# Kernel tuning notes

Hardware: AMD Instinct MI355X
Metric: run time of the kernel (lower is better)

Reference implementation:

```python
import jax, jax.numpy as jnp
import numpy as np

LEAKY_SLOPE = 0.01  # torch nn.LeakyReLU default

def _mlp(x, w1, b1, w2, b2):
    # MLP_Layer(num_layers=2, batch_norm=False): Linear -> ReLU -> Linear
    return jax.nn.relu(x @ w1 + b1) @ w2 + b2

def _edge_softmax(scores, dst, num_nodes):
    # softmax over incoming edges of each destination node; scores: [E, H]
    m = jax.ops.segment_max(scores, dst, num_segments=num_nodes)  # [N, H]
    e = jnp.exp(scores - m[dst])
    s = jax.ops.segment_sum(e, dst, num_segments=num_nodes)       # [N, H]
    return e / s[dst]

def setup_inputs() -> dict:
    key = jax.random.key(0)
    ks = jax.random.split(key, 10)
    N, E, H = 50000, 800000, 4
    D_H, PCA, PI, HID = 64, 64, 32, 128
    inp = {
        "h":    jax.random.normal(ks[0], (N, D_H), jnp.float32),
        "pca":  jax.random.normal(ks[1], (N, PCA), jnp.float32),
        "pimg": jax.random.normal(ks[2], (N, PI), jnp.float32),
        "pca_w1": jax.random.normal(ks[3], (2 * PCA, HID), jnp.float32) * (1.0 / np.sqrt(2 * PCA)),
        "pca_b1": jnp.zeros((HID,), jnp.float32),
        "pca_w2": jax.random.normal(ks[4], (HID, H), jnp.float32) * (1.0 / np.sqrt(HID)),
        "pca_b2": jnp.zeros((H,), jnp.float32),
        "pi_w1": jax.random.normal(ks[5], (2 * PI, HID), jnp.float32) * (1.0 / np.sqrt(2 * PI)),
        "pi_b1": jnp.zeros((HID,), jnp.float32),
        "pi_w2": jax.random.normal(ks[6], (HID, H), jnp.float32) * (1.0 / np.sqrt(HID)),
        "pi_b2": jnp.zeros((H,), jnp.float32),
        "src": jax.random.randint(ks[7], (E,), 0, N, jnp.int32),
        "dst": jax.random.randint(ks[8], (E,), 0, N, jnp.int32),
    }
    return inp

def reference(h, pca, pimg, pca_w1, pca_b1, pca_w2, pca_b2,
              pi_w1, pi_b1, pi_w2, pi_b2, src, dst):
    N = h.shape[0]

    def attend(feat, w1, b1, w2, b2):
        e_feat = jnp.concatenate([feat[src], feat[dst]], axis=1)        # [E, 2F]
        score = jax.nn.leaky_relu(_mlp(e_feat, w1, b1, w2, b2), LEAKY_SLOPE)  # [E, H]
        a = _edge_softmax(score, dst, N)                                # [E, H]
        msg = h[src][:, None, :] * a[:, :, None]                        # [E, H, D]
        return jax.ops.segment_sum(msg, dst, num_segments=N)           # [N, H, D]

    out_pca = attend(pca, pca_w1, pca_b1, pca_w2, pca_b2)
    out_pi = attend(pimg, pi_w1, pi_b1, pi_w2, pi_b2)
    return jnp.concatenate([out_pca, out_pi], axis=-1)                  # [N, H, 2D]
```

## Files before the change

### kernel.cpp

```cpp
#include <hip/hip_runtime.h>
#include <hip/hip_fp16.h>

constexpr int HID = 128;
constexpr int DH  = 64;

typedef _Float16 f16x2 __attribute__((ext_vector_type(2)));
typedef _Float16 fh8   __attribute__((ext_vector_type(8)));
typedef float    f32x4v __attribute__((ext_vector_type(4)));

__device__ __forceinline__ fh8 relu8(fh8 x) {
  fh8 z = {0, 0, 0, 0, 0, 0, 0, 0};
#if __has_builtin(__builtin_elementwise_max)
  return __builtin_elementwise_max(x, z);
#else
  fh8 r;
#pragma unroll
  for (int i = 0; i < 8; i++) r[i] = x[i] > z[i] ? x[i] : z[i];
  return r;
#endif
}

template<int F, int NB>
__launch_bounds__(256)
__global__ void uv_kernel(const float* __restrict__ feat, const float* __restrict__ w1,
                          const float* __restrict__ b1,
                          _Float16* __restrict__ u_cat, _Float16* __restrict__ v_cat,
                          int roff, int N) {
  __shared__ float sfeat[NB][F + 1];
  int nb = blockIdx.x * NB;
  for (int i = threadIdx.x; i < NB * F; i += 256) {
    int n = i / F, k = i - n * F;
    int gn = nb + n;
    sfeat[n][k] = (gn < N) ? feat[(size_t)gn * F + k] : 0.f;
  }
  __syncthreads();
  int j = threadIdx.x & 127;
  int g = threadIdx.x >> 7;
  constexpr int NPT = NB / 2;
  float ua[NPT], va[NPT];
#pragma unroll
  for (int i = 0; i < NPT; i++) { ua[i] = 0.f; va[i] = 0.f; }
  for (int k = 0; k < F; k++) {
    float wu = w1[k * HID + j];
    float wv = w1[(F + k) * HID + j];
#pragma unroll
    for (int i = 0; i < NPT; i++) {
      float f = sfeat[g * NPT + i][k];
      ua[i] = fmaf(f, wu, ua[i]);
      va[i] = fmaf(f, wv, va[i]);
    }
  }
  float b1v = b1[j];
#pragma unroll
  for (int i = 0; i < NPT; i++) {
    int gn = nb + g * NPT + i;
    if (gn < N) {
      u_cat[(size_t)gn * 256 + roff + j] = (_Float16)ua[i];
      v_cat[(size_t)gn * 256 + roff + j] = (_Float16)(va[i] + b1v);
    }
  }
}

__global__ void h16_kernel(const float* __restrict__ h, _Float16* __restrict__ h16, int total) {
  int i = (blockIdx.x * 256 + threadIdx.x) * 4;
  if (i + 3 < total) {
    float4 v = *(const float4*)(h + i);
    h16[i] = (_Float16)v.x; h16[i + 1] = (_Float16)v.y;
    h16[i + 2] = (_Float16)v.z; h16[i + 3] = (_Float16)v.w;
  } else {
    for (int q = 0; q < 4; q++) if (i + q < total) h16[i + q] = (_Float16)h[i + q];
  }
}

__global__ void count_kernel(const int* __restrict__ dst, int* __restrict__ counts, int E) {
  int e = blockIdx.x * 256 + threadIdx.x;
  if (e < E) atomicAdd(&counts[dst[e]], 1);
}

__launch_bounds__(256)
__global__ void scan1_kernel(const int* __restrict__ counts, int* __restrict__ bsums, int N) {
  int b = blockIdx.x, tid = threadIdx.x;
  int base = b * 1024 + tid * 4;
  int s = 0;
  if (base + 3 < N) {
    int4 v = *(const int4*)(counts + base);
    s = v.x + v.y + v.z + v.w;
  } else {
    for (int q = 0; q < 4; q++) { int idx = base + q; if (idx < N) s += counts[idx]; }
  }
#pragma unroll
  for (int o = 32; o >= 1; o >>= 1) s += __shfl_xor(s, o);
  __shared__ int ws[4];
  if ((tid & 63) == 0) ws[tid >> 6] = s;
  __syncthreads();
  if (tid == 0) bsums[b] = ws[0] + ws[1] + ws[2] + ws[3];
}

__launch_bounds__(1024)
__global__ void scan2_kernel(const int* __restrict__ bsums, int* __restrict__ bpre,
                             int* __restrict__ offsets, int NB, int N, int E) {
  int tid = threadIdx.x, lane = tid & 63, w = tid >> 6;
  int v = (tid < NB) ? bsums[tid] : 0;
  int incl = v;
#pragma unroll
  for (int o = 1; o < 64; o <<= 1) { int t = __shfl_up(incl, o); if (lane >= o) incl += t; }
  __shared__ int ws[16];
  if (lane == 63) ws[w] = incl;
  __syncthreads();
  int wpre = 0;
  for (int q = 0; q < w; q++) wpre += ws[q];
  if (tid < NB) bpre[tid] = wpre + incl - v;
  if (tid == 0) offsets[N] = E;
}

__launch_bounds__(256)
__global__ void scan3_kernel(const int* __restrict__ counts, const int* __restrict__ bpre,
                             int* __restrict__ offsets, int N) {
  int b = blockIdx.x, tid = threadIdx.x, lane = tid & 63, w = tid >> 6;
  int base = b * 1024 + tid * 4;
  int c[4] = {0, 0, 0, 0};
  if (base + 3 < N) {
    int4 v = *(const int4*)(counts + base);
    c[0] = v.x; c[1] = v.y; c[2] = v.z; c[3] = v.w;
  } else {
    for (int q = 0; q < 4; q++) { int idx = base + q; if (idx < N) c[q] = counts[idx]; }
  }
  int s = c[0] + c[1] + c[2] + c[3];
  int incl = s;
#pragma unroll
  for (int o = 1; o < 64; o <<= 1) { int t = __shfl_up(incl, o); if (lane >= o) incl += t; }
  int excl = incl - s;
  __shared__ int ws[4];
  if (lane == 63) ws[w] = incl;
  __syncthreads();
  int wpre = 0;
  for (int q = 0; q < w; q++) wpre += ws[q];
  int off = bpre[b] + wpre + excl;
  for (int q = 0; q < 4; q++) {
    int idx = base + q;
    if (idx < N) offsets[idx] = off;
    off += c[q];
  }
}

__global__ void fill_kernel(const int* __restrict__ src, const int* __restrict__ dst,
                            int* __restrict__ cursor, int2* __restrict__ edges, int E) {
  int e = blockIdx.x * 256 + threadIdx.x;
  if (e < E) {
    int d = dst[e];
    int pos = atomicAdd(&cursor[d], 1);
    edges[pos] = make_int2(src[e], d);
  }
}

__launch_bounds__(256, 8)
__global__ void score_kernel(const _Float16* __restrict__ u_cat, const _Float16* __restrict__ v_cat,
                             const int2* __restrict__ edges,
                             const float* __restrict__ w2a, const float* __restrict__ w2b,
                             const float* __restrict__ b2a, const float* __restrict__ b2b,
                             _Float16* __restrict__ ek, int E) {
  __shared__ _Float16 sB[8 * 64 * 8];
  int tid = threadIdx.x, lane = tid & 63, w = tid >> 6;
  int col = lane & 15, kg = lane >> 4;
  for (int idx = tid; idx < 4096; idx += 256) {
    int t = idx >> 9, l = (idx >> 3) & 63, j = idx & 7;
    int bc = l & 15;
    int k = t * 32 + ((l >> 4) << 3) + j;
    float val = 0.f;
    if (bc < 4) { if (k < 128) val = w2a[k * 4 + bc]; }
    else if (bc < 8) { if (k >= 128) val = w2b[(k - 128) * 4 + (bc - 4)]; }
    sB[idx] = (_Float16)val;
  }
  __syncthreads();

  int ebase = blockIdx.x * 256 + w * 64;

  const _Float16* up[4];
  const _Float16* vp[4];
#pragma unroll
  for (int m = 0; m < 4; m++) {
    int em = ebase + m * 16 + col;
    int ec = em < E ? em : 0;
    int2 sd = edges[ec];
    up[m] = u_cat + (size_t)sd.x * 256 + kg * 8;
    vp[m] = v_cat + (size_t)sd.y * 256 + kg * 8;
  }

  f32x4v acc[4];
#pragma unroll
  for (int m = 0; m < 4; m++) acc[m] = (f32x4v){0.f, 0.f, 0.f, 0.f};

#pragma unroll
  for (int t = 0; t < 8; t++) {
    fh8 bf = *(const fh8*)(sB + ((t * 64 + lane) << 3));
#pragma unroll
    for (int m = 0; m < 4; m++) {
      fh8 uu = *(const fh8*)(up[m] + t * 32);
      fh8 vv = *(const fh8*)(vp[m] + t * 32);
      acc[m] = __builtin_amdgcn_mfma_f32_16x16x32_f16(relu8(uu + vv), bf, acc[m], 0, 0, 0);
    }
  }

  if (col < 8) {
    float b2v = (col < 4) ? b2a[col] : b2b[col - 4];
#pragma unroll
    for (int m = 0; m < 4; m++) {
#pragma unroll
      for (int q = 0; q < 4; q++) {
        int er = ebase + m * 16 + kg * 4 + q;
        if (er < E) {
          float x = acc[m][q] + b2v;
          x = x > 0.f ? x : 0.01f * x;
          ek[(size_t)er * 8 + col] = (_Float16)__expf(x);
        }
      }
    }
  }
}

__launch_bounds__(256, 6)
__global__ void agg_kernel(const _Float16* __restrict__ ek, const int2* __restrict__ edges,
                           const int* __restrict__ offsets, const _Float16* __restrict__ h16,
                           float* __restrict__ out, int N) {
  int wid = blockIdx.x * 4 + (threadIdx.x >> 6);
  int lane = threadIdx.x & 63;
  if (wid >= N) return;
  int off0 = offsets[wid], off1 = offsets[wid + 1];
  int deg = off1 - off0;
  float* op = out + (size_t)wid * 512;
  if (deg == 0) {
#pragma unroll
    for (int k = 0; k < 4; k++) { op[k * 128 + lane] = 0.f; op[k * 128 + 64 + lane] = 0.f; }
    return;
  }
  float accO[8] = {0, 0, 0, 0, 0, 0, 0, 0};
  float ssum[8] = {0, 0, 0, 0, 0, 0, 0, 0};
  int last = off1 - 1;
  for (int jj = 0; jj < deg; jj += 4) {
    int i0 = off0 + jj;
    int i1 = min(i0 + 1, last), i2 = min(i0 + 2, last), i3 = min(i0 + 3, last);
    bool m1 = jj + 1 < deg, m2 = jj + 2 < deg, m3 = jj + 3 < deg;
    int s0 = edges[i0].x, s1 = edges[i1].x, s2 = edges[i2].x, s3 = edges[i3].x;
    fh8 e0 = *(const fh8*)(ek + (size_t)i0 * 8);
    fh8 e1 = *(const fh8*)(ek + (size_t)i1 * 8);
    fh8 e2 = *(const fh8*)(ek + (size_t)i2 * 8);
    fh8 e3 = *(const fh8*)(ek + (size_t)i3 * 8);
    float hv0 = (float)h16[(size_t)s0 * DH + lane];
    float hv1 = (float)h16[(size_t)s1 * DH + lane];
    float hv2 = (float)h16[(size_t)s2 * DH + lane];
    float hv3 = (float)h16[(size_t)s3 * DH + lane];
#pragma unroll
    for (int k = 0; k < 8; k++) {
      float e0v = (float)e0[k];
      float e1v = m1 ? (float)e1[k] : 0.f;
      float e2v = m2 ? (float)e2[k] : 0.f;
      float e3v = m3 ? (float)e3[k] : 0.f;
      accO[k] = fmaf(e0v, hv0, accO[k]);
      accO[k] = fmaf(e1v, hv1, accO[k]);
      accO[k] = fmaf(e2v, hv2, accO[k]);
      accO[k] = fmaf(e3v, hv3, accO[k]);
      ssum[k] += (e0v + e1v) + (e2v + e3v);
    }
  }
#pragma unroll
  for (int k = 0; k < 8; k++) {
    float rsv = 1.f / ssum[k];
    int colo = k < 4 ? k * 128 + lane : (k - 4) * 128 + 64 + lane;
    op[colo] = accO[k] * rsv;
  }
}

extern "C" void kernel_launch(void* const* d_in, const int* in_sizes, int n_in,
                              void* d_out, int out_size, void* d_ws, size_t ws_size,
                              hipStream_t stream) {
  const float* h      = (const float*)d_in[0];
  const float* pca    = (const float*)d_in[1];
  const float* pimg   = (const float*)d_in[2];
  const float* pca_w1 = (const float*)d_in[3];
  const float* pca_b1 = (const float*)d_in[4];
  const float* pca_w2 = (const float*)d_in[5];
  const float* pca_b2 = (const float*)d_in[6];
  const float* pi_w1  = (const float*)d_in[7];
  const float* pi_b1  = (const float*)d_in[8];
  const float* pi_w2  = (const float*)d_in[9];
  const float* pi_b2  = (const float*)d_in[10];
  const int*   src    = (const int*)d_in[11];
  const int*   dst    = (const int*)d_in[12];
  int N = in_sizes[0] / 64;
  int E = in_sizes[11];
  float* out = (float*)d_out;

  char* ws = (char*)d_ws;
  size_t o = 0;
  auto alloc = [&](size_t bytes) { void* p = ws + o; o += (bytes + 255) & ~(size_t)255; return p; };
  _Float16* u_cat = (_Float16*)alloc((size_t)N * 256 * 2);
  _Float16* v_cat = (_Float16*)alloc((size_t)N * 256 * 2);
  _Float16* h16   = (_Float16*)alloc((size_t)N * 64 * 2);
  int* counts  = (int*)alloc((size_t)N * 4);
  int* cursor  = (int*)alloc((size_t)N * 4);
  int* offsets = (int*)alloc((size_t)(N + 1) * 4);
  int* bsums   = (int*)alloc(1024 * 4);
  int* bpre    = (int*)alloc(1024 * 4);
  int2* edges  = (int2*)alloc((size_t)E * 8);
  _Float16* ekb = (_Float16*)alloc((size_t)E * 8 * 2);

  hipMemsetAsync(counts, 0, (size_t)N * 4, stream);

  uv_kernel<64, 32><<<(N + 31) / 32, 256, 0, stream>>>(pca, pca_w1, pca_b1, u_cat, v_cat, 0, N);
  uv_kernel<32, 32><<<(N + 31) / 32, 256, 0, stream>>>(pimg, pi_w1, pi_b1, u_cat, v_cat, 128, N);
  h16_kernel<<<((N * 64) / 4 + 255) / 256, 256, 0, stream>>>(h, h16, N * 64);
  count_kernel<<<(E + 255) / 256, 256, 0, stream>>>(dst, counts, E);
  int NB = (N + 1023) / 1024;
  scan1_kernel<<<NB, 256, 0, stream>>>(counts, bsums, N);
  scan2_kernel<<<1, 1024, 0, stream>>>(bsums, bpre, offsets, NB, N, E);
  scan3_kernel<<<NB, 256, 0, stream>>>(counts, bpre, offsets, N);
  hipMemcpyAsync(cursor, offsets, (size_t)N * 4, hipMemcpyDeviceToDevice, stream);
  fill_kernel<<<(E + 255) / 256, 256, 0, stream>>>(src, dst, cursor, edges, E);
  score_kernel<<<(E + 255) / 256, 256, 0, stream>>>(u_cat, v_cat, edges,
                                                    pca_w2, pi_w2, pca_b2, pi_b2, ekb, E);
  agg_kernel<<<(N + 3) / 4, 256, 0, stream>>>(ekb, edges, offsets, h16, out, N);
}
```

Baseline: 323.1 us.

## Compute node projections with MFMA and fuse degree counting with h conversion

Replaces the scalar FMA node projection kernels with one MFMA f16 kernel that handles both feature sets in a 2D grid. The weight fragments are prepared once by a small setup kernel. The edge-count and h-to-fp16 conversion kernels are merged into a single launch, and the aggregation kernel's launch bounds are raised to allow more resident blocks. This trades fp32 accumulation of the inputs for fp16 operands in the first layer and cuts launch count and scalar ALU work.

```diff
diff --git a/kernel.cpp b/kernel.cpp
--- a/kernel.cpp
+++ b/kernel.cpp
@@ -20,61 +20,95 @@
 #endif
 }
 
-template<int F, int NB>
+__global__ void frag_setup_kernel(const float* __restrict__ w1a, const float* __restrict__ w1b,
+                                  _Float16* __restrict__ fragTab) {
+  int flat = blockIdx.x * 256 + threadIdx.x;
+  if (flat >= 32768) return;
+  int rel = flat >> 14;
+  int r2 = flat & 16383;
+  int g = r2 >> 10, s = (r2 >> 9) & 1, l = (r2 >> 3) & 63, j = r2 & 7;
+  int bc = l & 15, bkg = l >> 4;
+  int k = s * 32 + bkg * 8 + j;
+  int F = rel ? 32 : 64;
+  const float* w1 = rel ? w1b : w1a;
+  float val = 0.f;
+  if (k < F) {
+    int jout = (g & 7) * 16 + bc;
+    int krow = (g < 8) ? k : (F + k);
+    val = w1[krow * HID + jout];
+  }
+  fragTab[flat] = (_Float16)val;
+}
+
 __launch_bounds__(256)
-__global__ void uv_kernel(const float* __restrict__ feat, const float* __restrict__ w1,
-                          const float* __restrict__ b1,
-                          _Float16* __restrict__ u_cat, _Float16* __restrict__ v_cat,
-                          int roff, int N) {
-  __shared__ float sfeat[NB][F + 1];
-  int nb = blockIdx.x * NB;
-  for (int i = threadIdx.x; i < NB * F; i += 256) {
-    int n = i / F, k = i - n * F;
-    int gn = nb + n;
-    sfeat[n][k] = (gn < N) ? feat[(size_t)gn * F + k] : 0.f;
-  }
-  __syncthreads();
-  int j = threadIdx.x & 127;
-  int g = threadIdx.x >> 7;
-  constexpr int NPT = NB / 2;
-  float ua[NPT], va[NPT];
-#pragma unroll
-  for (int i = 0; i < NPT; i++) { ua[i] = 0.f; va[i] = 0.f; }
-  for (int k = 0; k < F; k++) {
-    float wu = w1[k * HID + j];
-    float wv = w1[(F + k) * HID + j];
-#pragma unroll
-    for (int i = 0; i < NPT; i++) {
-      float f = sfeat[g * NPT + i][k];
-      ua[i] = fmaf(f, wu, ua[i]);
-      va[i] = fmaf(f, wv, va[i]);
-    }
-  }
-  float b1v = b1[j];
-#pragma unroll
-  for (int i = 0; i < NPT; i++) {
-    int gn = nb + g * NPT + i;
-    if (gn < N) {
-      u_cat[(size_t)gn * 256 + roff + j] = (_Float16)ua[i];
-      v_cat[(size_t)gn * 256 + roff + j] = (_Float16)(va[i] + b1v);
-    }
-  }
-}
-
-__global__ void h16_kernel(const float* __restrict__ h, _Float16* __restrict__ h16, int total) {
-  int i = (blockIdx.x * 256 + threadIdx.x) * 4;
-  if (i + 3 < total) {
-    float4 v = *(const float4*)(h + i);
-    h16[i] = (_Float16)v.x; h16[i + 1] = (_Float16)v.y;
-    h16[i + 2] = (_Float16)v.z; h16[i + 3] = (_Float16)v.w;
-  } else {
-    for (int q = 0; q < 4; q++) if (i + q < total) h16[i + q] = (_Float16)h[i + q];
-  }
-}
-
-__global__ void count_kernel(const int* __restrict__ dst, int* __restrict__ counts, int E) {
-  int e = blockIdx.x * 256 + threadIdx.x;
-  if (e < E) atomicAdd(&counts[dst[e]], 1);
+__global__ void uv_mfma_kernel(const float* __restrict__ pca, const float* __restrict__ pimg,
+                               const float* __restrict__ b1a, const float* __restrict__ b1b,
+                               const _Float16* __restrict__ fragTab,
+                               _Float16* __restrict__ u_cat, _Float16* __restrict__ v_cat, int N) {
+  __shared__ _Float16 sB[16384];
+  int rel = blockIdx.y;
+  const float* feat = rel ? pimg : pca;
+  const float* b1   = rel ? b1b : b1a;
+  int F  = rel ? 32 : 64;
+  int KS = rel ? 1 : 2;
+  int tid = threadIdx.x;
+  {
+    const fh8* srcp = (const fh8*)(fragTab + rel * 16384);
+    fh8* dstp = (fh8*)sB;
+    for (int i = tid; i < 2048; i += 256) dstp[i] = srcp[i];
+  }
+  __syncthreads();
+  int lane = tid & 63, w = tid >> 6;
+  int r = lane & 15, kg = lane >> 4;
+  int node = blockIdx.x * 64 + w * 16 + r;
+  int nclamp = node < N ? node : N - 1;
+  fh8 a[2];
+#pragma unroll
+  for (int s = 0; s < 2; s++) {
+    if (s < KS) {
+      const float* fp = feat + (size_t)nclamp * F + s * 32 + kg * 8;
+      float4 f0 = *(const float4*)fp;
+      float4 f1 = *(const float4*)(fp + 4);
+      fh8 t;
+      t[0] = (_Float16)f0.x; t[1] = (_Float16)f0.y; t[2] = (_Float16)f0.z; t[3] = (_Float16)f0.w;
+      t[4] = (_Float16)f1.x; t[5] = (_Float16)f1.y; t[6] = (_Float16)f1.z; t[7] = (_Float16)f1.w;
+      a[s] = t;
+    }
+  }
+  int onode0 = blockIdx.x * 64 + w * 16 + kg * 4;
+  int c = lane & 15;
+#pragma unroll
+  for (int g = 0; g < 16; g++) {
+    f32x4v acc = {0.f, 0.f, 0.f, 0.f};
+    acc = __builtin_amdgcn_mfma_f32_16x16x32_f16(a[0], ((const fh8*)sB)[(g * 2 + 0) * 64 + lane], acc, 0, 0, 0);
+    if (KS == 2)
+      acc = __builtin_amdgcn_mfma_f32_16x16x32_f16(a[1], ((const fh8*)sB)[(g * 2 + 1) * 64 + lane], acc, 0, 0, 0);
+    bool isv = g >= 8;
+    int jout = (g & 7) * 16 + c;
+    float bias = isv ? b1[jout] : 0.f;
+    _Float16* outp = isv ? v_cat : u_cat;
+    size_t colix = (size_t)rel * 128 + jout;
+#pragma unroll
+    for (int q = 0; q < 4; q++) {
+      int on = onode0 + q;
+      if (on < N) outp[(size_t)on * 256 + colix] = (_Float16)(acc[q] + bias);
+    }
+  }
+}
+
+__global__ void count_h16_kernel(const int* __restrict__ dst, int* __restrict__ counts, int E,
+                                 const float* __restrict__ h, _Float16* __restrict__ h16, int total) {
+  int i = blockIdx.x * 256 + threadIdx.x;
+  if (i < E) atomicAdd(&counts[dst[i]], 1);
+  int base = i * 8;
+  if (base + 7 < total) {
+    float4 f0 = *(const float4*)(h + base);
+    float4 f1 = *(const float4*)(h + base + 4);
+    fh8 t;
+    t[0] = (_Float16)f0.x; t[1] = (_Float16)f0.y; t[2] = (_Float16)f0.z; t[3] = (_Float16)f0.w;
+    t[4] = (_Float16)f1.x; t[5] = (_Float16)f1.y; t[6] = (_Float16)f1.z; t[7] = (_Float16)f1.w;
+    *(fh8*)(h16 + base) = t;
+  }
 }
 
 __launch_bounds__(256)
@@ -174,7 +208,6 @@
   __syncthreads();
 
   int ebase = blockIdx.x * 256 + w * 64;
-
   const _Float16* up[4];
   const _Float16* vp[4];
 #pragma unroll
@@ -218,7 +251,7 @@
   }
 }
 
-__launch_bounds__(256, 6)
+__launch_bounds__(256, 8)
 __global__ void agg_kernel(const _Float16* __restrict__ ek, const int2* __restrict__ edges,
                            const int* __restrict__ offsets, const _Float16* __restrict__ h16,
                            float* __restrict__ out, int N) {
@@ -293,9 +326,10 @@
   char* ws = (char*)d_ws;
   size_t o = 0;
   auto alloc = [&](size_t bytes) { void* p = ws + o; o += (bytes + 255) & ~(size_t)255; return p; };
-  _Float16* u_cat = (_Float16*)alloc((size_t)N * 256 * 2);
-  _Float16* v_cat = (_Float16*)alloc((size_t)N * 256 * 2);
-  _Float16* h16   = (_Float16*)alloc((size_t)N * 64 * 2);
+  _Float16* u_cat  = (_Float16*)alloc((size_t)N * 256 * 2);
+  _Float16* v_cat  = (_Float16*)alloc((size_t)N * 256 * 2);
+  _Float16* h16    = (_Float16*)alloc((size_t)N * 64 * 2);
+  _Float16* fragTab = (_Float16*)alloc(32768 * 2);
   int* counts  = (int*)alloc((size_t)N * 4);
   int* cursor  = (int*)alloc((size_t)N * 4);
   int* offsets = (int*)alloc((size_t)(N + 1) * 4);
@@ -306,10 +340,10 @@
 
   hipMemsetAsync(counts, 0, (size_t)N * 4, stream);
 
-  uv_kernel<64, 32><<<(N + 31) / 32, 256, 0, stream>>>(pca, pca_w1, pca_b1, u_cat, v_cat, 0, N);
-  uv_kernel<32, 32><<<(N + 31) / 32, 256, 0, stream>>>(pimg, pi_w1, pi_b1, u_cat, v_cat, 128, N);
-  h16_kernel<<<((N * 64) / 4 + 255) / 256, 256, 0, stream>>>(h, h16, N * 64);
-  count_kernel<<<(E + 255) / 256, 256, 0, stream>>>(dst, counts, E);
+  frag_setup_kernel<<<128, 256, 0, stream>>>(pca_w1, pi_w1, fragTab);
+  count_h16_kernel<<<(E + 255) / 256, 256, 0, stream>>>(dst, counts, E, h, h16, N * 64);
+  dim3 uvgrid((N + 63) / 64, 2);
+  uv_mfma_kernel<<<uvgrid, 256, 0, stream>>>(pca, pimg, pca_b1, pi_b1, fragTab, u_cat, v_cat, N);
   int NB = (N + 1023) / 1024;
   scan1_kernel<<<NB, 256, 0, stream>>>(counts, bsums, N);
   scan2_kernel<<<1, 1024, 0, stream>>>(bsums, bpre, offsets, NB, N, E);
```

Measured after the change: 290.1 us. 10.2% less time.
